# Performance work log

Measured on AMD Instinct MI355X. Metric: run time of the kernel, lower is better.

The kernel has to match this reference:

```python
import jax, jax.numpy as jnp
import numpy as np

N_NODES = 50000
N_EDGES = 800000
N_GRAPHS = 256
VOCAB = 40
EMB = 128
HID = 256
NCLS = 10


def setup_inputs() -> dict:
    key = jax.random.key(0)
    ks = jax.random.split(key, 12)
    x = jax.random.randint(ks[0], (N_NODES,), 0, VOCAB)
    edge_index = jax.random.randint(ks[1], (2, N_EDGES), 0, N_NODES)
    batch = jnp.sort(jax.random.randint(ks[2], (N_NODES,), 0, N_GRAPHS))

    def init(k, shape, fan_in):
        return jax.random.normal(k, shape, jnp.float32) * (1.0 / np.sqrt(fan_in))

    return {
        "x": x,
        "edge_index": edge_index,
        "batch": batch,
        "emb": init(ks[3], (VOCAB, EMB), EMB),
        "W1l": init(ks[4], (EMB, HID), EMB),
        "W1r": init(ks[5], (EMB, HID), EMB),
        "b1": jnp.zeros((HID,), jnp.float32),
        "W2l": init(ks[6], (HID, HID), HID),
        "W2r": init(ks[7], (HID, HID), HID),
        "b2": jnp.zeros((HID,), jnp.float32),
        "Wo": init(ks[8], (HID, NCLS), HID),
        "bo": jnp.zeros((NCLS,), jnp.float32),
    }


def _segment_mean(v, ids, n):
    # v: [M, D], ids: [M] -> [n, D] mean per segment (empty segments -> 0)
    s = jax.ops.segment_sum(v, ids, num_segments=n)
    c = jax.ops.segment_sum(jnp.ones((ids.shape[0], 1), v.dtype), ids, num_segments=n)
    return s / jnp.maximum(c, 1.0)


def _sage_conv(h, src, dst, Wl, Wr, b):
    # PyG SAGEConv: lin_l(mean of neighbor msgs) + lin_r(self) + bias
    mean_nb = _segment_mean(h[src], dst, h.shape[0])  # [N, D_in]
    return mean_nb @ Wl + h @ Wr + b


def reference(x, edge_index, batch, emb, W1l, W1r, b1, W2l, W2r, b2, Wo, bo):
    src, dst = edge_index[0], edge_index[1]
    h = emb[x]                                          # [N, EMB]
    h = jax.nn.relu(_sage_conv(h, src, dst, W1l, W1r, b1))  # [N, HID]
    h = jax.nn.relu(_sage_conv(h, src, dst, W2l, W2r, b2))  # [N, HID]
    g = _segment_mean(h, batch, N_GRAPHS)               # [G, HID]
    return g @ Wo + bo                                  # [G, NCLS]
```

## Files before the change

kernel.cpp:

```cpp
#include <hip/hip_runtime.h>
#include <hip/hip_bf16.h>

#define N_NODES 50000
#define N_GRAPHS 256
#define EMB 128
#define HID 256
#define NCLS 10
#define VOCAB 40
#define NPAD 50048
#define DMAX 64
#define NEDGE 800000

typedef __attribute__((ext_vector_type(4))) float f32x4;
typedef __attribute__((ext_vector_type(8))) _Float16 f16x8;
typedef __attribute__((ext_vector_type(4))) _Float16 f16x4;
typedef unsigned int u32;
#define AS1 __attribute__((address_space(1)))
#define AS3 __attribute__((address_space(3)))

__device__ __forceinline__ int imax(int a, int b) { return a > b ? a : b; }
__device__ __forceinline__ int imin(int a, int b) { return a < b ? a : b; }
__device__ __forceinline__ float bf2f(ushort h) { return __uint_as_float(((unsigned)h) << 16); }

__device__ __forceinline__ int detect_bf16(const unsigned short* w) {
    int ok = 1;
#pragma unroll
    for (int i = 0; i < 64; ++i) {
        float f = __uint_as_float(((unsigned)w[i]) << 16);
        ok &= (fabsf(f) < 16.0f) ? 1 : 0;
    }
    return ok;
}
__device__ __forceinline__ float ldw(const void* p, int idx, int bf) {
    if (bf) return bf2f(((const unsigned short*)p)[idx]);
    return ((const float*)p)[idx];
}


struct PrepArgs {
    const void* bsrc[4];
    const unsigned short* emb16;
    const void* W1l; const void* W1r;
    const void* W2l; const void* W2r;
    const int* batch;
    float* Wb;
    _Float16* W2t;
    _Float16* EWt;
    float* EW2;
    int* gstart;
    float* g_acc;
    int* deg;
};

__global__ void prep_k(PrepArgs a) {
    int b = blockIdx.x, t = threadIdx.x;
    if (b < 13) {
        int i = b * 256 + t;
        if (i < 3082) {
            int bf = detect_bf16(a.emb16);
            const int cum[5] = {0, 256, 512, 3072, 3082};
            int s = 0;
            while (i >= cum[s + 1]) ++s;
            a.Wb[i] = ldw(a.bsrc[s], i - cum[s], bf);
        }
    } else if (b < 525) {
        int bf = detect_bf16(a.emb16);
        int j = (b - 13) * 256 + t;
        int n = j >> 9, k = j & 511;
        const void* p = (k < 256) ? a.W2l : a.W2r;
        a.W2t[(size_t)n * 512 + k] = (_Float16)ldw(p, (k & 255) * 256 + n, bf);
    } else if (b < 589) {
        int v = b - 525, n = t;
        if (v >= VOCAB) { a.EWt[n * 64 + v] = (_Float16)0.f; return; }
        int bf = detect_bf16(a.emb16);
        float s1 = 0.f, s2 = 0.f;
        for (int k = 0; k < EMB; ++k) {
            float ev = ldw(a.emb16, v * EMB + k, bf);
            s1 = fmaf(ev, ldw(a.W1l, k * 256 + n, bf), s1);
            s2 = fmaf(ev, ldw(a.W1r, k * 256 + n, bf), s2);
        }
        a.EWt[n * 64 + v] = (_Float16)s1;
        a.EW2[v * 256 + n] = s2;
    } else if (b < 785) {
        int i = (b - 589) * 256 + t;
        if (i < N_NODES) {
            int bb = a.batch[i];
            int bp = (i == 0) ? -1 : a.batch[i - 1];
            for (int g = bp + 1; g <= bb; ++g) a.gstart[g] = i;
            if (i == N_NODES - 1)
                for (int g = bb + 1; g <= N_GRAPHS; ++g) a.gstart[g] = N_NODES;
        }
    } else if (b < 1041) {
        int i = (b - 785) * 256 + t;
        if (i < N_GRAPHS * HID) a.g_acc[i] = 0.f;
    } else {
        int i = (b - 1041) * 256 + t;
        if (i < N_NODES) a.deg[i] = 0;
    }
}

__global__ void scatter_k(const int* __restrict__ src, const int* __restrict__ dst,
                          int* __restrict__ deg, ushort* __restrict__ col) {
    int e = blockIdx.x * blockDim.x + threadIdx.x;
    if (e < NEDGE) {
        int d = dst[e];
        int p = atomicAdd(&deg[d], 1);
        if (p < DMAX) col[d * DMAX + p] = (ushort)src[e];
    }
}

__global__ __launch_bounds__(256, 2) void gemm1_k(
    const int* __restrict__ deg, const ushort* __restrict__ colv,
    const int* __restrict__ x, const _Float16* __restrict__ EWt,
    const float* __restrict__ EW2, const float* __restrict__ bias,
    char* __restrict__ E) {
    __shared__ ushort cnt[VOCAB * 256];
    __shared__ __attribute__((aligned(16))) char As[8192];
    const int tid = threadIdx.x, wave = tid >> 6, lane = tid & 63;
    const int row0 = blockIdx.x * 64, col0 = wave * 64;

    f16x8 B[8];
#pragma unroll
    for (int n = 0; n < 4; ++n) {
        const _Float16* wp = EWt + (size_t)(col0 + n * 16 + (lane & 15)) * 64 + ((lane >> 4) * 8);
        B[n] = *(const f16x8*)wp;
        B[4 + n] = *(const f16x8*)(wp + 32);
    }

    int nl = tid >> 2, sub = tid & 3;
    int n = row0 + nl;
#pragma unroll
    for (int v = 0; v < VOCAB; ++v) cnt[v * 256 + tid] = 0;
    __syncthreads();
    if (n < N_NODES) {
        int s0 = n * DMAX;
        int s1 = s0 + imin(deg[n], DMAX);
        for (int e = s0 + sub; e < s1; e += 4) {
            int v = x[colv[e]];
            cnt[v * 256 + tid]++;
        }
    }
    __syncthreads();
    if (tid < 64) {
        char* trow = As + tid * 128;
        int xorb = tid & 7;
#pragma unroll
        for (int b = 0; b < 8; ++b) {
            int kbase = (b ^ xorb) * 8;
            f16x8 o;
#pragma unroll
            for (int j = 0; j < 8; ++j) {
                int k = kbase + j;
                int c = 0;
                if (k < VOCAB)
                    c = cnt[k * 256 + tid * 4 + 0] + cnt[k * 256 + tid * 4 + 1] +
                        cnt[k * 256 + tid * 4 + 2] + cnt[k * 256 + tid * 4 + 3];
                o[j] = (_Float16)(float)c;
            }
            *(f16x8*)(trow + b * 16) = o;
        }
    }
    __syncthreads();

    int offA[2][4];
#pragma unroll
    for (int h = 0; h < 2; ++h)
#pragma unroll
        for (int m = 0; m < 4; ++m) {
            int r = (lane & 15) + m * 16;
            int b = h * 64 + (lane >> 4) * 16;
            offA[h][m] = r * 128 + (b ^ ((r & 7) << 4));
        }
    f32x4 acc[4][4];
#pragma unroll
    for (int m = 0; m < 4; ++m)
#pragma unroll
        for (int nn = 0; nn < 4; ++nn) acc[m][nn] = (f32x4){0.f, 0.f, 0.f, 0.f};
#pragma unroll
    for (int h = 0; h < 2; ++h) {
        f16x8 a[4];
#pragma unroll
        for (int m = 0; m < 4; ++m) a[m] = *(const f16x8*)(As + offA[h][m]);
#pragma unroll
        for (int m = 0; m < 4; ++m)
#pragma unroll
            for (int nn = 0; nn < 4; ++nn)
                acc[m][nn] = __builtin_amdgcn_mfma_f32_16x16x32_f16(a[m], B[h * 4 + nn],
                                                                    acc[m][nn], 0, 0, 0);
    }
    int rbase = row0 + ((lane >> 4) * 4);
    int cbase = col0 + (lane & 15);
    float bv[4];
#pragma unroll
    for (int nn = 0; nn < 4; ++nn) bv[nn] = bias[cbase + nn * 16];
#pragma unroll
    for (int m = 0; m < 4; ++m)
#pragma unroll
        for (int r = 0; r < 4; ++r) {
            int row = rbase + m * 16 + r;
            if (row < N_NODES) {
                float invd = 1.f / (float)imax(deg[row], 1);
                const float* e2 = EW2 + (size_t)x[row] * 256;
#pragma unroll
                for (int nn = 0; nn < 4; ++nn) {
                    int colc = cbase + nn * 16;
                    float v = acc[m][nn][r] * invd + e2[colc] + bv[nn];
                    v = v > 0.f ? v : 0.f;
                    char* ep = E + ((size_t)(row >> 6) * 8 + 4 + (colc >> 6)) * 8192 +
                               (row & 63) * 128 + (((colc & 63) * 2) ^ ((row & 7) << 4));
                    *(_Float16*)ep = (_Float16)v;
                }
            }
        }
}

__global__ void agg2_k(const int* __restrict__ deg, const ushort* __restrict__ colv,
                       char* __restrict__ A2c) {
    int w = (blockIdx.x * blockDim.x + threadIdx.x) >> 6;
    int lane = threadIdx.x & 63;
    if (w >= N_NODES) return;
    int dg = deg[w];
    int s0 = w * DMAX, s1 = s0 + imin(dg, DMAX);
    int ktof = 4 + (lane >> 4);
    int bof = (lane & 15) * 8;
    float ac0 = 0.f, ac1 = 0.f, ac2 = 0.f, ac3 = 0.f;
#define ADDR2(s) (A2c + ((size_t)((s) >> 6) * 8 + ktof) * 8192 + ((s) & 63) * 128 + \
                  (bof ^ (((s) & 7) << 4)))
    int e = s0;
    for (; e + 4 <= s1; e += 4) {
        int sA = colv[e], sB = colv[e + 1], sC = colv[e + 2], sD = colv[e + 3];
        f16x4 h0 = *(const f16x4*)ADDR2(sA);
        f16x4 h1 = *(const f16x4*)ADDR2(sB);
        f16x4 h2 = *(const f16x4*)ADDR2(sC);
        f16x4 h3 = *(const f16x4*)ADDR2(sD);
        ac0 += (float)h0[0] + (float)h1[0] + (float)h2[0] + (float)h3[0];
        ac1 += (float)h0[1] + (float)h1[1] + (float)h2[1] + (float)h3[1];
        ac2 += (float)h0[2] + (float)h1[2] + (float)h2[2] + (float)h3[2];
        ac3 += (float)h0[3] + (float)h1[3] + (float)h2[3] + (float)h3[3];
    }
    for (; e < s1; ++e) {
        f16x4 hv = *(const f16x4*)ADDR2(colv[e]);
        ac0 += (float)hv[0];
        ac1 += (float)hv[1];
        ac2 += (float)hv[2];
        ac3 += (float)hv[3];
    }
#undef ADDR2
    float inv = 1.f / (float)imax(dg, 1);
    f16x4 o;
    o[0] = (_Float16)(ac0 * inv);
    o[1] = (_Float16)(ac1 * inv);
    o[2] = (_Float16)(ac2 * inv);
    o[3] = (_Float16)(ac3 * inv);
    char* mp = A2c + ((size_t)(w >> 6) * 8 + (ktof - 4)) * 8192 + (w & 63) * 128 +
               (bof ^ ((w & 7) << 4));
    *(f16x4*)mp = o;
}

template <int K>
__global__ __launch_bounds__(256, 2) void gemm2_k(
    const char* __restrict__ Aswz, const _Float16* __restrict__ Wt,
    const float* __restrict__ bias, const int* __restrict__ batch,
    float* __restrict__ g_acc) {
    constexpr int NT = K / 64;
    __shared__ __attribute__((aligned(16))) char As[4 * 8192];
    const int tid = threadIdx.x, wave = tid >> 6, lane = tid & 63;
    const int row0 = blockIdx.x * 64, col0 = wave * 64;
    const char* Ab = Aswz + (size_t)blockIdx.x * NT * 8192 + tid * 16;
    const _Float16* Wp = Wt + (size_t)(col0 + (lane & 15)) * K + ((lane >> 4) * 8);

    int offA[2][4];
#pragma unroll
    for (int h = 0; h < 2; ++h)
#pragma unroll
        for (int m = 0; m < 4; ++m) {
            int r = (lane & 15) + m * 16;
            int b = h * 64 + (lane >> 4) * 16;
            offA[h][m] = r * 128 + (b ^ ((r & 7) << 4));
        }

    f32x4 acc[4][4];
#pragma unroll
    for (int m = 0; m < 4; ++m)
#pragma unroll
        for (int n = 0; n < 4; ++n) acc[m][n] = (f32x4){0.f, 0.f, 0.f, 0.f};

    f16x8 B0[8], B1[8];

#define STAGE(t)                                                                     \
    {                                                                                \
        const char* _s = Ab + (size_t)(t) * 8192;                                    \
        char* _d = As + ((t) & 3) * 8192 + tid * 16;                                 \
        __builtin_amdgcn_global_load_lds((const AS1 u32*)_s, (AS3 u32*)_d, 16, 0, 0);\
        __builtin_amdgcn_global_load_lds((const AS1 u32*)(_s + 4096),                \
                                         (AS3 u32*)(_d + 4096), 16, 0, 0);           \
    }
#define LOADB(t, Bf)                                                                 \
    {                                                                                \
        _Pragma("unroll") for (int n = 0; n < 4; ++n) {                              \
            Bf[n]     = *(const f16x8*)(Wp + (size_t)n * 16 * K + (t) * 64);         \
            Bf[4 + n] = *(const f16x8*)(Wp + (size_t)n * 16 * K + (t) * 64 + 32);    \
        }                                                                            \
    }
#define COMP(p, Bf)                                                                  \
    {                                                                                \
        const char* _b = As + (p) * 8192;                                            \
        _Pragma("unroll") for (int h = 0; h < 2; ++h) {                              \
            f16x8 _a[4];                                                             \
            _Pragma("unroll") for (int m = 0; m < 4; ++m)                            \
                _a[m] = *(const f16x8*)(_b + offA[h][m]);                            \
            _Pragma("unroll") for (int m = 0; m < 4; ++m)                            \
                _Pragma("unroll") for (int n = 0; n < 4; ++n)                        \
                    acc[m][n] = __builtin_amdgcn_mfma_f32_16x16x32_f16(              \
                        _a[m], Bf[h * 4 + n], acc[m][n], 0, 0, 0);                   \
        }                                                                            \
    }
#define WAITBAR()                                                                    \
    {                                                                                \
        asm volatile("s_waitcnt vmcnt(12)" ::: "memory");                            \
        __builtin_amdgcn_s_barrier();                                                \
        asm volatile("" ::: "memory");                                               \
    }

    STAGE(0);
    LOADB(0, B0);
    STAGE(1);
    STAGE(2);

#pragma unroll 1
    for (int t = 0; t < NT; t += 2) {
        WAITBAR();
        if (t + 3 < NT) STAGE(t + 3);
        LOADB(t + 1, B1);
        COMP(t & 3, B0);
        WAITBAR();
        if (t + 4 < NT) STAGE(t + 4);
        if (t + 2 < NT) LOADB(t + 2, B0);
        COMP((t + 1) & 3, B1);
    }

    __syncthreads();
    float bv[4];
#pragma unroll
    for (int n = 0; n < 4; ++n) bv[n] = bias[col0 + n * 16 + (lane & 15)];
    int rloc = (lane >> 4) * 4;
    int cbase = col0 + (lane & 15);
#pragma unroll
    for (int m = 0; m < 4; ++m)
#pragma unroll
        for (int n = 0; n < 4; ++n)
#pragma unroll
            for (int r = 0; r < 4; ++r) {
                float v = acc[m][n][r] + bv[n];
                v = v > 0.f ? v : 0.f;
                *(_Float16*)(As + (rloc + m * 16 + r) * 512 + (cbase + n * 16) * 2) =
                    (_Float16)v;
            }
    __syncthreads();
    int rmax = imin(64, N_NODES - row0);
    int cur = batch[row0];
    float run = 0.f;
    for (int r = 0; r < rmax; ++r) {
        int b = batch[row0 + r];
        if (b != cur) {
            atomicAdd(&g_acc[cur * HID + tid], run);
            run = 0.f;
            cur = b;
        }
        run += (float)*(const _Float16*)(As + r * 512 + tid * 2);
    }
    atomicAdd(&g_acc[cur * HID + tid], run);
#undef STAGE
#undef LOADB
#undef COMP
#undef WAITBAR
}

__global__ void final_k(const float* __restrict__ g_acc, const int* __restrict__ gstart,
                        const float* __restrict__ Wo, const float* __restrict__ bo,
                        void* __restrict__ out, const unsigned short* __restrict__ emb16) {
    __shared__ float gm[HID];
    __shared__ float red[HID];
    int g = blockIdx.x, t = threadIdx.x;
    int cnt = gstart[g + 1] - gstart[g];
    float inv = 1.0f / (float)imax(cnt, 1);
    gm[t] = g_acc[g * HID + t] * inv;
    __syncthreads();
    int bf = detect_bf16(emb16);
    for (int c = 0; c < NCLS; ++c) {
        red[t] = gm[t] * Wo[t * NCLS + c];
        __syncthreads();
        for (int s = HID / 2; s > 0; s >>= 1) {
            if (t < s) red[t] += red[t + s];
            __syncthreads();
        }
        if (t == 0) {
            float o = red[0] + bo[c];
            if (bf) ((__hip_bfloat16*)out)[g * NCLS + c] = __float2bfloat16(o);
            else    ((float*)out)[g * NCLS + c] = o;
        }
        __syncthreads();
    }
}

extern "C" void kernel_launch(void* const* d_in, const int* in_sizes, int n_in,
                              void* d_out, int out_size, void* d_ws, size_t ws_size,
                              hipStream_t stream) {
    const int* x     = (const int*)d_in[0];
    const int* ei    = (const int*)d_in[1];
    const int* batch = (const int*)d_in[2];
    const int* srcp = ei;
    const int* dstp = ei + NEDGE;

    char* w = (char*)d_ws;
    auto alloc = [&](size_t bytes) -> char* {
        char* p = w;
        w += (bytes + 255) & ~(size_t)255;
        return p;
    };
    float* g_acc = (float*)alloc((size_t)N_GRAPHS * HID * 4);
    int* deg     = (int*)alloc((size_t)N_NODES * 4);
    int* gstart  = (int*)alloc((size_t)(N_GRAPHS + 1) * 4);
    ushort* col  = (ushort*)alloc((size_t)N_NODES * DMAX * 2);
    float* Wb    = (float*)alloc((size_t)3328 * 4);
    _Float16* W2t = (_Float16*)alloc((size_t)256 * 512 * 2);
    _Float16* EWt = (_Float16*)alloc((size_t)256 * 64 * 2);
    float* EW2    = (float*)alloc((size_t)VOCAB * 256 * 4);
    char* A2c     = alloc((size_t)(NPAD / 64) * 8 * 8192);
    alloc(4096);

    PrepArgs pa;
    pa.bsrc[0] = d_in[6];  pa.bsrc[1] = d_in[9];
    pa.bsrc[2] = d_in[10]; pa.bsrc[3] = d_in[11];
    pa.emb16 = (const unsigned short*)d_in[3];
    pa.W1l = d_in[4]; pa.W1r = d_in[5];
    pa.W2l = d_in[7]; pa.W2r = d_in[8];
    pa.batch = batch;
    pa.Wb = Wb; pa.W2t = W2t; pa.EWt = EWt; pa.EW2 = EW2;
    pa.gstart = gstart; pa.g_acc = g_acc; pa.deg = deg;
    prep_k<<<1237, 256, 0, stream>>>(pa);

    scatter_k<<<(NEDGE + 255) / 256, 256, 0, stream>>>(srcp, dstp, deg, col);

    const int GB = NPAD / 64;
    gemm1_k<<<GB, 256, 0, stream>>>(deg, col, x, EWt, EW2, Wb, A2c);
    agg2_k<<<(N_NODES * 64 + 255) / 256, 256, 0, stream>>>(deg, col, A2c);
    gemm2_k<512><<<GB, 256, 0, stream>>>(A2c, W2t, Wb + 256, batch, g_acc);
    final_k<<<N_GRAPHS, HID, 0, stream>>>(g_acc, gstart, Wb + 512, Wb + 3072, d_out,
                                          (const unsigned short*)d_in[3]);

    (void)in_sizes; (void)n_in; (void)out_size; (void)ws_size;
}
```

Before: 208.9 us.

## Merge prep and edge scatter, split vocab counting from layer-1 GEMM

Zeroing of g_acc and deg moves to a single memset ahead of the prep work. The edge scatter becomes extra blocks of the prep kernel, which removes one launch. The per-node vocabulary histogram moves out of gemm1 into its own kernel that writes a swizzled count tile to global memory. gemm1 then loads that tile straight into LDS with global_load_lds, so the GEMM no longer needs the large LDS histogram, which may let more blocks fit per CU. The agg2 gather loop is unrolled to 8 loads in flight. In exchange this adds a memset, an extra kernel launch and a global round trip for the counts tile.

```diff
diff --git a/kernel.cpp b/kernel.cpp
--- a/kernel.cpp
+++ b/kernel.cpp
@@ -10,6 +10,8 @@
 #define NPAD 50048
 #define DMAX 64
 #define NEDGE 800000
+#define PREPB 785
+#define SCB 3125
 
 typedef __attribute__((ext_vector_type(4))) float f32x4;
 typedef __attribute__((ext_vector_type(8))) _Float16 f16x8;
@@ -37,7 +39,9 @@
 }
 
 
-struct PrepArgs {
+struct BuildArgs {
+    const int* src; const int* dst;
+    int* deg; ushort* col;
     const void* bsrc[4];
     const unsigned short* emb16;
     const void* W1l; const void* W1r;
@@ -48,12 +52,20 @@
     _Float16* EWt;
     float* EW2;
     int* gstart;
-    float* g_acc;
-    int* deg;
 };
 
-__global__ void prep_k(PrepArgs a) {
-    int b = blockIdx.x, t = threadIdx.x;
+__global__ void build_k(BuildArgs a) {
+    int bid = blockIdx.x, t = threadIdx.x;
+    if (bid >= PREPB) {
+        int e = (bid - PREPB) * 256 + t;
+        if (e < NEDGE) {
+            int d = a.dst[e];
+            int p = atomicAdd(&a.deg[d], 1);
+            if (p < DMAX) a.col[d * DMAX + p] = (ushort)a.src[e];
+        }
+        return;
+    }
+    int b = bid;
     if (b < 13) {
         int i = b * 256 + t;
         if (i < 3082) {
@@ -81,7 +93,7 @@
         }
         a.EWt[n * 64 + v] = (_Float16)s1;
         a.EW2[v * 256 + n] = s2;
-    } else if (b < 785) {
+    } else {
         int i = (b - 589) * 256 + t;
         if (i < N_NODES) {
             int bb = a.batch[i];
@@ -90,48 +102,17 @@
             if (i == N_NODES - 1)
                 for (int g = bb + 1; g <= N_GRAPHS; ++g) a.gstart[g] = N_NODES;
         }
-    } else if (b < 1041) {
-        int i = (b - 785) * 256 + t;
-        if (i < N_GRAPHS * HID) a.g_acc[i] = 0.f;
-    } else {
-        int i = (b - 1041) * 256 + t;
-        if (i < N_NODES) a.deg[i] = 0;
-    }
-}
-
-__global__ void scatter_k(const int* __restrict__ src, const int* __restrict__ dst,
-                          int* __restrict__ deg, ushort* __restrict__ col) {
-    int e = blockIdx.x * blockDim.x + threadIdx.x;
-    if (e < NEDGE) {
-        int d = dst[e];
-        int p = atomicAdd(&deg[d], 1);
-        if (p < DMAX) col[d * DMAX + p] = (ushort)src[e];
-    }
-}
-
-__global__ __launch_bounds__(256, 2) void gemm1_k(
-    const int* __restrict__ deg, const ushort* __restrict__ colv,
-    const int* __restrict__ x, const _Float16* __restrict__ EWt,
-    const float* __restrict__ EW2, const float* __restrict__ bias,
-    char* __restrict__ E) {
+    }
+}
+
+__global__ void ct2_k(const int* __restrict__ deg, const ushort* __restrict__ colv,
+                      const int* __restrict__ x, char* __restrict__ Ct) {
     __shared__ ushort cnt[VOCAB * 256];
-    __shared__ __attribute__((aligned(16))) char As[8192];
-    const int tid = threadIdx.x, wave = tid >> 6, lane = tid & 63;
-    const int row0 = blockIdx.x * 64, col0 = wave * 64;
-
-    f16x8 B[8];
-#pragma unroll
-    for (int n = 0; n < 4; ++n) {
-        const _Float16* wp = EWt + (size_t)(col0 + n * 16 + (lane & 15)) * 64 + ((lane >> 4) * 8);
-        B[n] = *(const f16x8*)wp;
-        B[4 + n] = *(const f16x8*)(wp + 32);
-    }
-
+    int tid = threadIdx.x;
     int nl = tid >> 2, sub = tid & 3;
-    int n = row0 + nl;
+    int n = blockIdx.x * 64 + nl;
 #pragma unroll
     for (int v = 0; v < VOCAB; ++v) cnt[v * 256 + tid] = 0;
-    __syncthreads();
     if (n < N_NODES) {
         int s0 = n * DMAX;
         int s1 = s0 + imin(deg[n], DMAX);
@@ -142,8 +123,9 @@
     }
     __syncthreads();
     if (tid < 64) {
-        char* trow = As + tid * 128;
-        int xorb = tid & 7;
+        int nn = blockIdx.x * 64 + tid;
+        char* tile = Ct + (size_t)(nn >> 6) * 8192 + (nn & 63) * 128;
+        int xorb = nn & 7;
 #pragma unroll
         for (int b = 0; b < 8; ++b) {
             int kbase = (b ^ xorb) * 8;
@@ -157,11 +139,30 @@
                         cnt[k * 256 + tid * 4 + 2] + cnt[k * 256 + tid * 4 + 3];
                 o[j] = (_Float16)(float)c;
             }
-            *(f16x8*)(trow + b * 16) = o;
-        }
-    }
-    __syncthreads();
-
+            *(f16x8*)(tile + b * 16) = o;
+        }
+    }
+}
+
+__global__ __launch_bounds__(256, 2) void gemm1_k(
+    const char* __restrict__ Ct, const _Float16* __restrict__ EWt,
+    const float* __restrict__ EW2, const int* __restrict__ xv,
+    const int* __restrict__ deg, const float* __restrict__ bias,
+    char* __restrict__ E) {
+    __shared__ __attribute__((aligned(16))) char As[8192];
+    const int tid = threadIdx.x, wave = tid >> 6, lane = tid & 63;
+    const int row0 = blockIdx.x * 64, col0 = wave * 64;
+    const char* sp = Ct + (size_t)blockIdx.x * 8192 + tid * 16;
+    __builtin_amdgcn_global_load_lds((const AS1 u32*)sp, (AS3 u32*)(As + tid * 16), 16, 0, 0);
+    __builtin_amdgcn_global_load_lds((const AS1 u32*)(sp + 4096),
+                                     (AS3 u32*)(As + tid * 16 + 4096), 16, 0, 0);
+    f16x8 B[8];
+#pragma unroll
+    for (int n = 0; n < 4; ++n) {
+        const _Float16* wp = EWt + (size_t)(col0 + n * 16 + (lane & 15)) * 64 + ((lane >> 4) * 8);
+        B[n] = *(const f16x8*)wp;
+        B[4 + n] = *(const f16x8*)(wp + 32);
+    }
     int offA[2][4];
 #pragma unroll
     for (int h = 0; h < 2; ++h)
@@ -175,7 +176,9 @@
 #pragma unroll
     for (int m = 0; m < 4; ++m)
 #pragma unroll
-        for (int nn = 0; nn < 4; ++nn) acc[m][nn] = (f32x4){0.f, 0.f, 0.f, 0.f};
+        for (int n = 0; n < 4; ++n) acc[m][n] = (f32x4){0.f, 0.f, 0.f, 0.f};
+    asm volatile("s_waitcnt vmcnt(0)" ::: "memory");
+    __syncthreads();
 #pragma unroll
     for (int h = 0; h < 2; ++h) {
         f16x8 a[4];
@@ -184,15 +187,15 @@
 #pragma unroll
         for (int m = 0; m < 4; ++m)
 #pragma unroll
-            for (int nn = 0; nn < 4; ++nn)
-                acc[m][nn] = __builtin_amdgcn_mfma_f32_16x16x32_f16(a[m], B[h * 4 + nn],
-                                                                    acc[m][nn], 0, 0, 0);
+            for (int n = 0; n < 4; ++n)
+                acc[m][n] = __builtin_amdgcn_mfma_f32_16x16x32_f16(a[m], B[h * 4 + n],
+                                                                   acc[m][n], 0, 0, 0);
     }
     int rbase = row0 + ((lane >> 4) * 4);
     int cbase = col0 + (lane & 15);
     float bv[4];
 #pragma unroll
-    for (int nn = 0; nn < 4; ++nn) bv[nn] = bias[cbase + nn * 16];
+    for (int n = 0; n < 4; ++n) bv[n] = bias[cbase + n * 16];
 #pragma unroll
     for (int m = 0; m < 4; ++m)
 #pragma unroll
@@ -200,11 +203,11 @@
             int row = rbase + m * 16 + r;
             if (row < N_NODES) {
                 float invd = 1.f / (float)imax(deg[row], 1);
-                const float* e2 = EW2 + (size_t)x[row] * 256;
-#pragma unroll
-                for (int nn = 0; nn < 4; ++nn) {
-                    int colc = cbase + nn * 16;
-                    float v = acc[m][nn][r] * invd + e2[colc] + bv[nn];
+                const float* e2 = EW2 + (size_t)xv[row] * 256;
+#pragma unroll
+                for (int n = 0; n < 4; ++n) {
+                    int colc = cbase + n * 16;
+                    float v = acc[m][n][r] * invd + e2[colc] + bv[n];
                     v = v > 0.f ? v : 0.f;
                     char* ep = E + ((size_t)(row >> 6) * 8 + 4 + (colc >> 6)) * 8192 +
                                (row & 63) * 128 + (((colc & 63) * 2) ^ ((row & 7) << 4));
@@ -227,19 +230,33 @@
 #define ADDR2(s) (A2c + ((size_t)((s) >> 6) * 8 + ktof) * 8192 + ((s) & 63) * 128 + \
                   (bof ^ (((s) & 7) << 4)))
     int e = s0;
-    for (; e + 4 <= s1; e += 4) {
-        int sA = colv[e], sB = colv[e + 1], sC = colv[e + 2], sD = colv[e + 3];
-        f16x4 h0 = *(const f16x4*)ADDR2(sA);
-        f16x4 h1 = *(const f16x4*)ADDR2(sB);
-        f16x4 h2 = *(const f16x4*)ADDR2(sC);
-        f16x4 h3 = *(const f16x4*)ADDR2(sD);
-        ac0 += (float)h0[0] + (float)h1[0] + (float)h2[0] + (float)h3[0];
-        ac1 += (float)h0[1] + (float)h1[1] + (float)h2[1] + (float)h3[1];
-        ac2 += (float)h0[2] + (float)h1[2] + (float)h2[2] + (float)h3[2];
-        ac3 += (float)h0[3] + (float)h1[3] + (float)h2[3] + (float)h3[3];
+    for (; e + 8 <= s1; e += 8) {
+        f16x4 hv[8];
+#pragma unroll
+        for (int j = 0; j < 8; ++j) hv[j] = *(const f16x4*)ADDR2((int)colv[e + j]);
+#pragma unroll
+        for (int j = 0; j < 8; ++j) {
+            ac0 += (float)hv[j][0];
+            ac1 += (float)hv[j][1];
+            ac2 += (float)hv[j][2];
+            ac3 += (float)hv[j][3];
+        }
+    }
+    if (e + 4 <= s1) {
+        f16x4 hv[4];
+#pragma unroll
+        for (int j = 0; j < 4; ++j) hv[j] = *(const f16x4*)ADDR2((int)colv[e + j]);
+#pragma unroll
+        for (int j = 0; j < 4; ++j) {
+            ac0 += (float)hv[j][0];
+            ac1 += (float)hv[j][1];
+            ac2 += (float)hv[j][2];
+            ac3 += (float)hv[j][3];
+        }
+        e += 4;
     }
     for (; e < s1; ++e) {
-        f16x4 hv = *(const f16x4*)ADDR2(colv[e]);
+        f16x4 hv = *(const f16x4*)ADDR2((int)colv[e]);
         ac0 += (float)hv[0];
         ac1 += (float)hv[1];
         ac2 += (float)hv[2];
@@ -426,24 +443,27 @@
     _Float16* W2t = (_Float16*)alloc((size_t)256 * 512 * 2);
     _Float16* EWt = (_Float16*)alloc((size_t)256 * 64 * 2);
     float* EW2    = (float*)alloc((size_t)VOCAB * 256 * 4);
+    char* Ct      = alloc((size_t)(NPAD / 64) * 8192);
     char* A2c     = alloc((size_t)(NPAD / 64) * 8 * 8192);
     alloc(4096);
 
-    PrepArgs pa;
-    pa.bsrc[0] = d_in[6];  pa.bsrc[1] = d_in[9];
-    pa.bsrc[2] = d_in[10]; pa.bsrc[3] = d_in[11];
-    pa.emb16 = (const unsigned short*)d_in[3];
-    pa.W1l = d_in[4]; pa.W1r = d_in[5];
-    pa.W2l = d_in[7]; pa.W2r = d_in[8];
-    pa.batch = batch;
-    pa.Wb = Wb; pa.W2t = W2t; pa.EWt = EWt; pa.EW2 = EW2;
-    pa.gstart = gstart; pa.g_acc = g_acc; pa.deg = deg;
-    prep_k<<<1237, 256, 0, stream>>>(pa);
-
-    scatter_k<<<(NEDGE + 255) / 256, 256, 0, stream>>>(srcp, dstp, deg, col);
+    hipMemsetAsync(g_acc, 0, (size_t)N_GRAPHS * HID * 4 + (size_t)N_NODES * 4, stream);
+
+    BuildArgs ba;
+    ba.src = srcp; ba.dst = dstp; ba.deg = deg; ba.col = col;
+    ba.bsrc[0] = d_in[6];  ba.bsrc[1] = d_in[9];
+    ba.bsrc[2] = d_in[10]; ba.bsrc[3] = d_in[11];
+    ba.emb16 = (const unsigned short*)d_in[3];
+    ba.W1l = d_in[4]; ba.W1r = d_in[5];
+    ba.W2l = d_in[7]; ba.W2r = d_in[8];
+    ba.batch = batch;
+    ba.Wb = Wb; ba.W2t = W2t; ba.EWt = EWt; ba.EW2 = EW2;
+    ba.gstart = gstart;
+    build_k<<<PREPB + SCB, 256, 0, stream>>>(ba);
 
     const int GB = NPAD / 64;
-    gemm1_k<<<GB, 256, 0, stream>>>(deg, col, x, EWt, EW2, Wb, A2c);
+    ct2_k<<<GB, 256, 0, stream>>>(deg, col, x, Ct);
+    gemm1_k<<<GB, 256, 0, stream>>>(Ct, EWt, EW2, x, deg, Wb, A2c);
     agg2_k<<<(N_NODES * 64 + 255) / 256, 256, 0, stream>>>(deg, col, A2c);
     gemm2_k<512><<<GB, 256, 0, stream>>>(A2c, W2t, Wb + 256, batch, g_acc);
     final_k<<<N_GRAPHS, HID, 0, stream>>>(g_acc, gstart, Wb + 512, Wb + 3072, d_out,
```

Result: slower. 216.0 us (+3.4%).
